# Kernel optimization log

Measured on AMD Instinct MI355X. Metric: run time of the kernel, lower is better.

## Reference

```python
import jax, jax.numpy as jnp
import numpy as np

NUM_GRAPHS = 512

def _segment_softmax(logits, seg, n):
    m = jax.ops.segment_max(logits, seg, num_segments=n)
    e = jnp.exp(logits - m[seg])
    z = jax.ops.segment_sum(e, seg, num_segments=n)
    return e / (z[seg] + 1e-16)

def _gat(x_src, x_dst, W_src, W_dst, a_src, a_dst, bias, src, dst, n_dst, n_loop):
    # PyG GATConv (concat=True, eval-mode dropout, self-loops added with
    # num_nodes = min(N_src, N_dst); inputs are guaranteed self-loop-free).
    H, C = a_src.shape
    hs = (x_src @ W_src).reshape(-1, H, C)  # [Ns,H,C]
    hd = (x_dst @ W_dst).reshape(-1, H, C)  # [Nd,H,C]
    als = jnp.einsum('nhc,hc->nh', hs, a_src)
    ald = jnp.einsum('nhc,hc->nh', hd, a_dst)
    loop = jnp.arange(n_loop)
    s = jnp.concatenate([src, loop])
    d = jnp.concatenate([dst, loop])
    logits = jax.nn.leaky_relu(als[s] + ald[d], 0.2)  # [E,H]
    alpha = _segment_softmax(logits, d, n_dst)
    out = jax.ops.segment_sum(hs[s] * alpha[:, :, None], d, num_segments=n_dst)
    return out.reshape(-1, H * C) + bias

def _graph_layernorm(x, batch, w, b, eps=1e-5):
    # PyG LayerNorm(mode='graph'): normalize over all nodes+features per graph.
    F = x.shape[-1]
    cnt = jax.ops.segment_sum(jnp.ones((x.shape[0],), x.dtype), batch, num_segments=NUM_GRAPHS)
    norm = jnp.maximum(cnt, 1.0) * F
    mean = jax.ops.segment_sum(x.sum(-1), batch, num_segments=NUM_GRAPHS) / norm
    xc = x - mean[batch][:, None]
    var = jax.ops.segment_sum((xc * xc).sum(-1), batch, num_segments=NUM_GRAPHS) / norm
    return xc * jax.lax.rsqrt(var + eps)[batch][:, None] * w + b

def _sag_pool(x, src, dst, batch, Wrel, brel, Wroot):
    # SAGPooling(min_score=-1): GraphConv score -> per-graph softmax; softmax>0>-1
    # so all nodes kept in order, x scaled by score.
    agg = jax.ops.segment_sum(x[src], dst, num_segments=x.shape[0])
    score = (agg @ Wrel + brel + x @ Wroot).reshape(-1)
    score = _segment_softmax(score, batch, NUM_GRAPHS)
    return x * score[:, None]

def setup_inputs() -> dict:
    key = jax.random.key(0)
    ks = jax.random.split(key, 32)
    N_ATOM, N_AA, B = 25600, 204800, 512
    E_ATOM, E_AA, E_M2P = 102400, 1024000, 512000
    D, H, C = 200, 2, 50
    HC = H * C
    sa = jax.random.randint(ks[0], (E_ATOM,), 0, N_ATOM)
    atom_edge_index = jnp.stack([sa, (sa + jax.random.randint(ks[1], (E_ATOM,), 1, N_ATOM)) % N_ATOM])
    sp = jax.random.randint(ks[2], (E_AA,), 0, N_AA)
    aa_edge_index = jnp.stack([sp, (sp + jax.random.randint(ks[3], (E_AA,), 1, N_AA)) % N_AA])
    m0 = jax.random.randint(ks[4], (E_M2P,), 0, N_ATOM)
    m1 = jax.random.randint(ks[5], (E_M2P,), 0, N_AA)
    m1 = jnp.where(m1 == m0, (m1 + 1) % N_AA, m1)  # keep bipartite edges self-loop-free
    m2p_edge_index = jnp.stack([m0, m1])
    f = lambda k, shape: jax.random.normal(k, shape, jnp.float32) * 0.05
    return dict(
        atom_x=jax.random.normal(ks[8], (N_ATOM, D)),
        atom_edge_index=atom_edge_index,
        atom_batch=jnp.sort(jax.random.randint(ks[6], (N_ATOM,), 0, B)),
        aa_x=jax.random.normal(ks[9], (N_AA, D)),
        aa_edge_index=aa_edge_index,
        aa_edge_attr=jax.random.uniform(ks[10], (E_AA, 1)),
        aa_batch=jnp.sort(jax.random.randint(ks[7], (N_AA,), 0, B)),
        m2p_edge_index=m2p_edge_index,
        Wd=f(ks[11], (D, HC)), ad_src=f(ks[12], (H, C)), ad_dst=f(ks[13], (H, C)), bd=jnp.zeros((HC,)),
        Wp=f(ks[14], (D, HC)), ap_src=f(ks[15], (H, C)), ap_dst=f(ks[16], (H, C)), bp=jnp.zeros((HC,)),
        Wi_src=f(ks[17], (D, HC)), Wi_dst=f(ks[18], (D, HC)), ai_src=f(ks[19], (H, C)), ai_dst=f(ks[20], (H, C)), bi=jnp.zeros((HC,)),
        ln_d_w=jnp.ones((D,)), ln_d_b=jnp.zeros((D,)),
        ln_p_w=jnp.ones((D,)), ln_p_b=jnp.zeros((D,)),
        pd_Wrel=f(ks[21], (D, 1)), pd_brel=jnp.zeros((1,)), pd_Wroot=f(ks[22], (D, 1)),
        pp_Wrel=f(ks[23], (D, 1)), pp_brel=jnp.zeros((1,)), pp_Wroot=f(ks[24], (D, 1)),
    )

def reference(atom_x, atom_edge_index, atom_batch, aa_x, aa_edge_index, aa_edge_attr, aa_batch, m2p_edge_index,
              Wd, ad_src, ad_dst, bd, Wp, ap_src, ap_dst, bp,
              Wi_src, Wi_dst, ai_src, ai_dst, bi,
              ln_d_w, ln_d_b, ln_p_w, ln_p_b,
              pd_Wrel, pd_brel, pd_Wroot, pp_Wrel, pp_brel, pp_Wroot):
    n_atom, n_aa = atom_x.shape[0], aa_x.shape[0]
    n_loop = min(n_atom, n_aa)
    atom_x = jax.nn.elu(atom_x)
    aa_x = jax.nn.elu(aa_x)
    # drug intra + inter (m2p flipped: src=aa, dst=atom)
    atom_intra = _gat(atom_x, atom_x, Wd, Wd, ad_src, ad_dst, bd,
                      atom_edge_index[0], atom_edge_index[1], n_atom, n_atom)
    atom_inter = _gat(aa_x, atom_x, Wi_src, Wi_dst, ai_src, ai_dst, bi,
                      m2p_edge_index[1], m2p_edge_index[0], n_atom, n_loop)
    atom_h = jax.nn.elu(_graph_layernorm(jnp.concatenate([atom_intra, atom_inter], -1), atom_batch, ln_d_w, ln_d_b))
    # protein intra + inter (uses UPDATED atom features; aa_edge_attr ignored: GATConv has no edge_dim)
    aa_intra = _gat(aa_x, aa_x, Wp, Wp, ap_src, ap_dst, bp,
                    aa_edge_index[0], aa_edge_index[1], n_aa, n_aa)
    aa_inter = _gat(atom_h, aa_x, Wi_src, Wi_dst, ai_src, ai_dst, bi,
                    m2p_edge_index[0], m2p_edge_index[1], n_aa, n_loop)
    aa_h = jax.nn.elu(_graph_layernorm(jnp.concatenate([aa_intra, aa_inter], -1), aa_batch, ln_p_w, ln_p_b))
    atom_out = _sag_pool(atom_h, atom_edge_index[0], atom_edge_index[1], atom_batch, pd_Wrel, pd_brel, pd_Wroot)
    aa_out = _sag_pool(aa_h, aa_edge_index[0], aa_edge_index[1], aa_batch, pp_Wrel, pp_brel, pp_Wroot)
    drug_g = jax.ops.segment_sum(atom_out, atom_batch, num_segments=NUM_GRAPHS)
    prot_g = jax.ops.segment_sum(aa_out, aa_batch, num_segments=NUM_GRAPHS)
    return atom_out, aa_out, drug_g, prot_g
```

## Files before the change

kernel.cpp:

```cpp
#include <hip/hip_runtime.h>

#define DF 200
#define HC 100
#define NH 2
#define CD 50
#define NG 512
#define SCB 256

__device__ __forceinline__ float eluf(float x){ return x>0.f ? x : expm1f(x); }

__device__ __forceinline__ void fma4(float4& a, float s, const float4& w){
  a.x += s*w.x; a.y += s*w.y; a.z += s*w.z; a.w += s*w.w;
}

__device__ __forceinline__ void seg_range(const int* __restrict__ batch, int N, int g,
                                          int& start, int& end){
  int lo=0, hi=N;
  while(lo<hi){ int m=(lo+hi)>>1; if(batch[m]<g) lo=m+1; else hi=m; }
  start=lo; hi=N;
  while(lo<hi){ int m=(lo+hi)>>1; if(batch[m]<g+1) lo=m+1; else hi=m; }
  end=lo;
}

__global__ void k_hist(const int* __restrict__ dst, int E, int* __restrict__ deg){
  int e = blockIdx.x*blockDim.x + threadIdx.x;
  if(e<E) atomicAdd(&deg[dst[e]], 1);
}

__global__ void k_scan1(int* __restrict__ a, int N, int* __restrict__ bsum){
  __shared__ int sh[SCB];
  int t = threadIdx.x, i = blockIdx.x*SCB + t;
  int v = (i<N)? a[i] : 0;
  sh[t] = v; __syncthreads();
  for(int o=1;o<SCB;o<<=1){
    int u = (t>=o)? sh[t-o] : 0; __syncthreads();
    sh[t] += u; __syncthreads();
  }
  if(i<N) a[i] = sh[t]-v;
  if(t==SCB-1) bsum[blockIdx.x] = sh[t];
}

__global__ void k_scan2(int* __restrict__ bsum, int nb){
  __shared__ int sh[1024];
  int t = threadIdx.x;
  int v = (t<nb)? bsum[t] : 0;
  sh[t]=v; __syncthreads();
  for(int o=1;o<1024;o<<=1){ int u=(t>=o)?sh[t-o]:0; __syncthreads(); sh[t]+=u; __syncthreads(); }
  if(t<nb) bsum[t] = sh[t]-v;
}

__global__ void k_scan3(int* __restrict__ rowptr, int* __restrict__ cursor,
                        const int* __restrict__ bsum, int N, int E){
  int i = blockIdx.x*SCB + threadIdx.x;
  if(i<N){ int v = rowptr[i] + bsum[blockIdx.x]; rowptr[i]=v; cursor[i]=v; }
  if(blockIdx.x==0 && threadIdx.x==0) rowptr[N]=E;
}

__global__ void k_fill(const int* __restrict__ src, const int* __restrict__ dst, int E,
                       int* __restrict__ cursor, int* __restrict__ csrc){
  int e = blockIdx.x*blockDim.x + threadIdx.x;
  if(e<E){ int p = atomicAdd(&cursor[dst[e]],1); csrc[p] = src[e]; }
}

__global__ void k_elu(const float* __restrict__ in, float* __restrict__ out, int n){
  int i = blockIdx.x*blockDim.x + threadIdx.x;
  if(i<n) out[i] = eluf(in[i]);
}

__global__ void k_makeV(const float* __restrict__ W, const float* __restrict__ a, float* __restrict__ V){
  int i = blockIdx.x*blockDim.x + threadIdx.x;
  if(i >= DF*NH) return;
  int k = i>>1, h = i&1;
  float s = 0.f;
  #pragma unroll
  for(int c=0;c<CD;c++) s += W[k*HC + h*CD + c] * a[h*CD + c];
  V[k*2+h] = s;
}

__global__ void k_pack2(const float* __restrict__ a, const float* __restrict__ c, float* __restrict__ V){
  int k = blockIdx.x*blockDim.x + threadIdx.x;
  if(k<DF){ V[k*2] = a[k]; V[k*2+1] = c[k]; }
}

__global__ void k_gemv3(const float* __restrict__ X,
                        const float* __restrict__ V0, const float* __restrict__ V1, const float* __restrict__ V2,
                        float* __restrict__ o0, float* __restrict__ o1, float* __restrict__ o2, int N){
  int n = blockIdx.x*4 + (threadIdx.x>>6);
  if(n>=N) return;
  int lane = threadIdx.x & 63;
  const float2* xr = (const float2*)(X + (size_t)n*DF);
  float a00=0,a01=0,a10=0,a11=0,a20=0,a21=0;
  for(int k2=lane;k2<DF/2;k2+=64){
    float2 x2 = xr[k2];
    float4 v0 = ((const float4*)V0)[k2];
    float4 v1 = ((const float4*)V1)[k2];
    float4 v2 = ((const float4*)V2)[k2];
    a00 += x2.x*v0.x + x2.y*v0.z;  a01 += x2.x*v0.y + x2.y*v0.w;
    a10 += x2.x*v1.x + x2.y*v1.z;  a11 += x2.x*v1.y + x2.y*v1.w;
    a20 += x2.x*v2.x + x2.y*v2.z;  a21 += x2.x*v2.y + x2.y*v2.w;
  }
  for(int o=32;o;o>>=1){
    a00+=__shfl_down(a00,o); a01+=__shfl_down(a01,o);
    a10+=__shfl_down(a10,o); a11+=__shfl_down(a11,o);
    a20+=__shfl_down(a20,o); a21+=__shfl_down(a21,o);
  }
  if(lane==0){
    o0[n*2]=a00; o0[n*2+1]=a01;
    o1[n*2]=a10; o1[n*2+1]=a11;
    o2[n*2]=a20; o2[n*2+1]=a21;
  }
}

__global__ void k_gemv4(const float* __restrict__ X,
                        const float* __restrict__ V0, const float* __restrict__ V1,
                        const float* __restrict__ V2, const float* __restrict__ V3,
                        float* __restrict__ o0, float* __restrict__ o1,
                        float* __restrict__ o2, float* __restrict__ o3, int N){
  int n = blockIdx.x*4 + (threadIdx.x>>6);
  if(n>=N) return;
  int lane = threadIdx.x & 63;
  const float2* xr = (const float2*)(X + (size_t)n*DF);
  float a00=0,a01=0,a10=0,a11=0,a20=0,a21=0,a30=0,a31=0;
  for(int k2=lane;k2<DF/2;k2+=64){
    float2 x2 = xr[k2];
    float4 v0 = ((const float4*)V0)[k2];
    float4 v1 = ((const float4*)V1)[k2];
    float4 v2 = ((const float4*)V2)[k2];
    float4 v3 = ((const float4*)V3)[k2];
    a00 += x2.x*v0.x + x2.y*v0.z;  a01 += x2.x*v0.y + x2.y*v0.w;
    a10 += x2.x*v1.x + x2.y*v1.z;  a11 += x2.x*v1.y + x2.y*v1.w;
    a20 += x2.x*v2.x + x2.y*v2.z;  a21 += x2.x*v2.y + x2.y*v2.w;
    a30 += x2.x*v3.x + x2.y*v3.z;  a31 += x2.x*v3.y + x2.y*v3.w;
  }
  for(int o=32;o;o>>=1){
    a00+=__shfl_down(a00,o); a01+=__shfl_down(a01,o);
    a10+=__shfl_down(a10,o); a11+=__shfl_down(a11,o);
    a20+=__shfl_down(a20,o); a21+=__shfl_down(a21,o);
    a30+=__shfl_down(a30,o); a31+=__shfl_down(a31,o);
  }
  if(lane==0){
    o0[n*2]=a00; o0[n*2+1]=a01;
    o1[n*2]=a10; o1[n*2+1]=a11;
    o2[n*2]=a20; o2[n*2+1]=a21;
    o3[n*2]=a30; o3[n*2+1]=a31;
  }
}

__global__ void k_gemm(const float* __restrict__ X, const float* __restrict__ W,
                       float* __restrict__ out, int N){
  int i = blockIdx.x*blockDim.x + threadIdx.x;
  int nq4 = (N+3)>>2;
  if(i >= nq4*25) return;
  int nq = i/25, cg = i%25;
  int n0 = nq*4;
  int r1 = min(n0+1,N-1), r2 = min(n0+2,N-1), r3 = min(n0+3,N-1);
  const float* x0 = X + (size_t)n0*DF;
  const float* x1 = X + (size_t)r1*DF;
  const float* x2 = X + (size_t)r2*DF;
  const float* x3 = X + (size_t)r3*DF;
  const float* wp = W + cg*4;
  float4 a0={0,0,0,0}, a1={0,0,0,0}, a2={0,0,0,0}, a3={0,0,0,0};
  for(int k=0;k<DF;k+=4){
    float4 xa = *(const float4*)(x0 + k);
    float4 xb = *(const float4*)(x1 + k);
    float4 xc = *(const float4*)(x2 + k);
    float4 xd = *(const float4*)(x3 + k);
    float4 w0 = *(const float4*)(wp + (k  )*HC);
    float4 w1 = *(const float4*)(wp + (k+1)*HC);
    float4 w2 = *(const float4*)(wp + (k+2)*HC);
    float4 w3 = *(const float4*)(wp + (k+3)*HC);
    fma4(a0,xa.x,w0); fma4(a0,xa.y,w1); fma4(a0,xa.z,w2); fma4(a0,xa.w,w3);
    fma4(a1,xb.x,w0); fma4(a1,xb.y,w1); fma4(a1,xb.z,w2); fma4(a1,xb.w,w3);
    fma4(a2,xc.x,w0); fma4(a2,xc.y,w1); fma4(a2,xc.z,w2); fma4(a2,xc.w,w3);
    fma4(a3,xd.x,w0); fma4(a3,xd.y,w1); fma4(a3,xd.z,w2); fma4(a3,xd.w,w3);
  }
  float* o = out + (size_t)n0*HC + cg*4;
  *(float4*)(o) = a0;
  if(n0+1<N) *(float4*)(o+HC)   = a1;
  if(n0+2<N) *(float4*)(o+2*HC) = a2;
  if(n0+3<N) *(float4*)(o+3*HC) = a3;
}

__global__ void k_gemm2(const float* __restrict__ X,
                        const float* __restrict__ W1, const float* __restrict__ W2,
                        float* __restrict__ out1, float* __restrict__ out2, int N){
  int i = blockIdx.x*blockDim.x + threadIdx.x;
  int nq4 = (N+3)>>2;
  if(i >= nq4*25) return;
  int nq = i/25, cg = i%25;
  int n0 = nq*4;
  int r1 = min(n0+1,N-1), r2 = min(n0+2,N-1), r3 = min(n0+3,N-1);
  const float* x0 = X + (size_t)n0*DF;
  const float* x1 = X + (size_t)r1*DF;
  const float* x2 = X + (size_t)r2*DF;
  const float* x3 = X + (size_t)r3*DF;
  const float* wp1 = W1 + cg*4;
  const float* wp2 = W2 + cg*4;
  float4 a0={0,0,0,0}, a1={0,0,0,0}, a2={0,0,0,0}, a3={0,0,0,0};
  float4 b0={0,0,0,0}, b1={0,0,0,0}, b2={0,0,0,0}, b3={0,0,0,0};
  for(int k=0;k<DF;k+=4){
    float4 xa = *(const float4*)(x0 + k);
    float4 xb = *(const float4*)(x1 + k);
    float4 xc = *(const float4*)(x2 + k);
    float4 xd = *(const float4*)(x3 + k);
    float4 u0 = *(const float4*)(wp1 + (k  )*HC);
    float4 u1 = *(const float4*)(wp1 + (k+1)*HC);
    float4 u2 = *(const float4*)(wp1 + (k+2)*HC);
    float4 u3 = *(const float4*)(wp1 + (k+3)*HC);
    float4 v0 = *(const float4*)(wp2 + (k  )*HC);
    float4 v1 = *(const float4*)(wp2 + (k+1)*HC);
    float4 v2 = *(const float4*)(wp2 + (k+2)*HC);
    float4 v3 = *(const float4*)(wp2 + (k+3)*HC);
    fma4(a0,xa.x,u0); fma4(a0,xa.y,u1); fma4(a0,xa.z,u2); fma4(a0,xa.w,u3);
    fma4(a1,xb.x,u0); fma4(a1,xb.y,u1); fma4(a1,xb.z,u2); fma4(a1,xb.w,u3);
    fma4(a2,xc.x,u0); fma4(a2,xc.y,u1); fma4(a2,xc.z,u2); fma4(a2,xc.w,u3);
    fma4(a3,xd.x,u0); fma4(a3,xd.y,u1); fma4(a3,xd.z,u2); fma4(a3,xd.w,u3);
    fma4(b0,xa.x,v0); fma4(b0,xa.y,v1); fma4(b0,xa.z,v2); fma4(b0,xa.w,v3);
    fma4(b1,xb.x,v0); fma4(b1,xb.y,v1); fma4(b1,xb.z,v2); fma4(b1,xb.w,v3);
    fma4(b2,xc.x,v0); fma4(b2,xc.y,v1); fma4(b2,xc.z,v2); fma4(b2,xc.w,v3);
    fma4(b3,xd.x,v0); fma4(b3,xd.y,v1); fma4(b3,xd.z,v2); fma4(b3,xd.w,v3);
  }
  float* o1 = out1 + (size_t)n0*HC + cg*4;
  float* o2 = out2 + (size_t)n0*HC + cg*4;
  *(float4*)(o1) = a0;
  *(float4*)(o2) = b0;
  if(n0+1<N){ *(float4*)(o1+HC)   = a1; *(float4*)(o2+HC)   = b1; }
  if(n0+2<N){ *(float4*)(o1+2*HC) = a2; *(float4*)(o2+2*HC) = b2; }
  if(n0+3<N){ *(float4*)(o1+3*HC) = a3; *(float4*)(o2+3*HC) = b3; }
}

__global__ void k_gat_gather(const int* __restrict__ rowptr, const int* __restrict__ csrc,
                             const float* __restrict__ hs,
                             const float* __restrict__ als, const float* __restrict__ ald,
                             const float* __restrict__ bias,
                             float* __restrict__ cat, int colOff, int nloop, int N){
  int n = blockIdx.x; if(n>=N) return;
  int f = threadIdx.x; if(f>=HC) return;
  int h = f/CD;
  float aldh = ald[n*2+h];
  float bi_f = bias[f];
  float acc = 0.f, z = 0.f;
  int e = rowptr[n], e1 = rowptr[n+1];
  for(; e<e1; e++){
    int s = csrc[e];
    float lg = als[s*2+h] + aldh;
    lg = lg>0.f ? lg : 0.2f*lg;
    float ev = __expf(lg);
    z += ev;
    acc += ev*hs[(size_t)s*HC+f];
  }
  if(n<nloop){
    float lg = als[n*2+h] + aldh;
    lg = lg>0.f ? lg : 0.2f*lg;
    float ev = __expf(lg);
    z += ev;
    acc += ev*hs[(size_t)n*HC+f];
  }
  cat[(size_t)n*DF + colOff + f] = acc/(z+1e-16f) + bi_f;
}

__global__ void k_ln_stats2(const float* __restrict__ cat, const int* __restrict__ batch,
                            float* __restrict__ gs, float* __restrict__ gq, float* __restrict__ gc, int N){
  int g = blockIdx.x, start, end;
  seg_range(batch, N, g, start, end);
  const float4* c4 = (const float4*)cat;
  int i0 = start*(DF/4), i1 = end*(DF/4);
  float s=0.f, q=0.f;
  for(int i=i0+threadIdx.x; i<i1; i+=blockDim.x){
    float4 v = c4[i];
    s += v.x+v.y+v.z+v.w;
    q += v.x*v.x+v.y*v.y+v.z*v.z+v.w*v.w;
  }
  for(int o=32;o;o>>=1){ s+=__shfl_down(s,o); q+=__shfl_down(q,o); }
  __shared__ float ss[8], sq[8];
  int wv = threadIdx.x>>6;
  if((threadIdx.x&63)==0){ ss[wv]=s; sq[wv]=q; }
  __syncthreads();
  if(threadIdx.x==0){
    float S=0.f, Q=0.f;
    int nw = blockDim.x>>6;
    for(int k=0;k<nw;k++){ S+=ss[k]; Q+=sq[k]; }
    gs[g]=S; gq[g]=Q; gc[g]=(float)(end-start);
  }
}

__global__ void k_ln_norm_f(float* __restrict__ x, const int* __restrict__ batch,
                            const float* __restrict__ gs, const float* __restrict__ gq, const float* __restrict__ gc,
                            const float* __restrict__ wv, const float* __restrict__ bv,
                            const float* __restrict__ V0, float* __restrict__ o0,
                            const float* __restrict__ V1, float* __restrict__ o1, int N){
  int n = blockIdx.x*4 + (threadIdx.x>>6);
  if(n>=N) return;
  int lane = threadIdx.x & 63;
  int g = batch[n];
  float norm = fmaxf(gc[g],1.f)*(float)DF;
  float mean = gs[g]/norm;
  float var  = fmaxf(gq[g]/norm - mean*mean, 0.f);
  float rs   = rsqrtf(var+1e-5f);
  float2* xr = (float2*)(x + (size_t)n*DF);
  float a00=0,a01=0,a10=0,a11=0;
  for(int k2=lane;k2<DF/2;k2+=64){
    float2 x2 = xr[k2];
    float2 w2 = ((const float2*)wv)[k2];
    float2 b2 = ((const float2*)bv)[k2];
    float v0 = eluf((x2.x-mean)*rs*w2.x + b2.x);
    float v1 = eluf((x2.y-mean)*rs*w2.y + b2.y);
    xr[k2] = make_float2(v0,v1);
    float4 vv = ((const float4*)V0)[k2];
    a00 += v0*vv.x + v1*vv.z;  a01 += v0*vv.y + v1*vv.w;
    if(V1){
      float4 u = ((const float4*)V1)[k2];
      a10 += v0*u.x + v1*u.z;  a11 += v0*u.y + v1*u.w;
    }
  }
  for(int o=32;o;o>>=1){
    a00+=__shfl_down(a00,o); a01+=__shfl_down(a01,o);
    a10+=__shfl_down(a10,o); a11+=__shfl_down(a11,o);
  }
  if(lane==0){
    o0[n*2]=a00; o0[n*2+1]=a01;
    if(o1){ o1[n*2]=a10; o1[n*2+1]=a11; }
  }
}

__global__ void k_sag_gather(const int* __restrict__ rowptr, const int* __restrict__ csrc,
                             const float* __restrict__ y2, float* __restrict__ sagg, int N){
  int n = blockIdx.x*blockDim.x + threadIdx.x;
  if(n>=N) return;
  float s=0.f;
  int e1 = rowptr[n+1];
  for(int e=rowptr[n]; e<e1; e++) s += y2[csrc[e]*2];
  sagg[n] = s;
}

__global__ void k_sag_exp(const float* __restrict__ sagg, const float* __restrict__ y2,
                          const float* __restrict__ brel,
                          float* __restrict__ en, float* __restrict__ zg,
                          const int* __restrict__ batch, int N){
  int n = blockIdx.x*blockDim.x + threadIdx.x;
  if(n>=N) return;
  float sc = sagg[n] + brel[0] + y2[n*2+1];
  float e = __expf(sc);
  en[n] = e;
  atomicAdd(&zg[batch[n]], e);
}

__global__ void k_sag_out(const float* __restrict__ x, const float* __restrict__ en,
                          const float* __restrict__ zg, const int* __restrict__ batch,
                          float* __restrict__ out, int N){
  int i = blockIdx.x*blockDim.x + threadIdx.x;
  if(i>=N*DF) return;
  int n = i/DF;
  float a = en[n]/(zg[batch[n]]+1e-16f);
  out[i] = x[i]*a;
}

__global__ void k_graph_sum(const float* __restrict__ x, const float* __restrict__ en,
                            const float* __restrict__ zg, const int* __restrict__ batch,
                            float* __restrict__ outg, int N){
  int g = blockIdx.x, start, end;
  seg_range(batch, N, g, start, end);
  int f = threadIdx.x;
  if(f>=DF) return;
  float s = 0.f;
  int n = start;
  for(; n+4<=end; n+=4){
    s += x[(size_t) n   *DF+f]*en[n]
       + x[(size_t)(n+1)*DF+f]*en[n+1]
       + x[(size_t)(n+2)*DF+f]*en[n+2]
       + x[(size_t)(n+3)*DF+f]*en[n+3];
  }
  for(; n<end; n++) s += x[(size_t)n*DF+f]*en[n];
  outg[(size_t)g*DF+f] = s/(zg[g]+1e-16f);
}

extern "C" void kernel_launch(void* const* d_in, const int* in_sizes, int n_in,
                              void* d_out, int out_size, void* d_ws, size_t ws_size,
                              hipStream_t stream){
  const float* atom_x    = (const float*)d_in[0];
  const int*   atom_ei   = (const int*)  d_in[1];
  const int*   atom_batch= (const int*)  d_in[2];
  const float* aa_x      = (const float*)d_in[3];
  const int*   aa_ei     = (const int*)  d_in[4];
  const int*   aa_batch  = (const int*)  d_in[6];
  const int*   m2p       = (const int*)  d_in[7];
  const float* Wd     =(const float*)d_in[8];
  const float* ad_src =(const float*)d_in[9];
  const float* ad_dst =(const float*)d_in[10];
  const float* bd     =(const float*)d_in[11];
  const float* Wp     =(const float*)d_in[12];
  const float* ap_src =(const float*)d_in[13];
  const float* ap_dst =(const float*)d_in[14];
  const float* bp     =(const float*)d_in[15];
  const float* Wi_src =(const float*)d_in[16];
  const float* Wi_dst =(const float*)d_in[17];
  const float* ai_src =(const float*)d_in[18];
  const float* ai_dst =(const float*)d_in[19];
  const float* bi     =(const float*)d_in[20];
  const float* ln_d_w =(const float*)d_in[21];
  const float* ln_d_b =(const float*)d_in[22];
  const float* ln_p_w =(const float*)d_in[23];
  const float* ln_p_b =(const float*)d_in[24];
  const float* pd_Wrel=(const float*)d_in[25];
  const float* pd_brel=(const float*)d_in[26];
  const float* pd_Wroot=(const float*)d_in[27];
  const float* pp_Wrel=(const float*)d_in[28];
  const float* pp_brel=(const float*)d_in[29];
  const float* pp_Wroot=(const float*)d_in[30];

  const int nA = in_sizes[0]/DF;
  const int EA = in_sizes[1]/2;
  const int nP = in_sizes[3]/DF;
  const int EP = in_sizes[4]/2;
  const int EM = in_sizes[7]/2;
  const int nLoop = nA<nP ? nA : nP;

  float* w = (float*)d_ws;
  size_t off = 0;
  auto alloc = [&](size_t n){ float* p = w+off; off += (n+63)&~(size_t)63; return p; };

  float* AX  = alloc((size_t)nA*DF);
  float* AB  = alloc((size_t)nP*DF);
  float* H1  = alloc((size_t)nA*HC);
  float* HS2 = alloc((size_t)nP*HC);
  float* H3  = alloc((size_t)nP*HC);
  float* als1=alloc((size_t)nA*2); float* ald1=alloc((size_t)nA*2);
  float* als2=alloc((size_t)nP*2); float* ald2=alloc((size_t)nA*2);
  float* als3=alloc((size_t)nP*2); float* ald3=alloc((size_t)nP*2);
  float* als4=alloc((size_t)nA*2); float* ald4=alloc((size_t)nP*2);
  float* Vds=alloc(DF*2); float* Vdd=alloc(DF*2);
  float* Vps=alloc(DF*2); float* Vpd=alloc(DF*2);
  float* Vis=alloc(DF*2); float* Vid=alloc(DF*2);
  float* VsA=alloc(DF*2); float* VsP=alloc(DF*2);
  float* y2A=alloc((size_t)nA*2); float* y2P=alloc((size_t)nP*2);
  float* enA=alloc(nA);   float* enP=alloc(nP);
  float* gsA=alloc(NG); float* gqA=alloc(NG); float* gcA=alloc(NG);
  float* gsP=alloc(NG); float* gqP=alloc(NG); float* gcP=alloc(NG);
  float* saggA=alloc(nA); float* saggP=alloc(nP);
  int* srcAi = (int*)alloc(EA);
  int* srcAm = (int*)alloc(EM);
  int* srcPi = (int*)alloc(EP);
  int* srcPm = (int*)alloc(EM);
  int* curAi = (int*)alloc(nA); int* curAm = (int*)alloc(nA);
  int* curPi = (int*)alloc(nP); int* curPm = (int*)alloc(nP);
  int* bsum  = (int*)alloc(1024);
  float* zr0 = w+off;
  int* rpAi = (int*)alloc(nA+1); int* rpAm = (int*)alloc(nA+1);
  int* rpPi = (int*)alloc(nP+1); int* rpPm = (int*)alloc(nP+1);
  float* zgA=alloc(NG); float* zgP=alloc(NG);
  size_t zrBytes = ((w+off) - zr0)*sizeof(float);
  if(off*sizeof(float) > ws_size) return;

  float* out_atom = (float*)d_out;
  float* out_aa   = out_atom + (size_t)nA*DF;
  float* out_dg   = out_aa   + (size_t)nP*DF;
  float* out_pg   = out_dg   + (size_t)NG*DF;

  const int B = 256;
  hipMemsetAsync(zr0, 0, zrBytes, stream);

  auto buildCSR = [&](const int* esrc, const int* edst, int E, int N,
                      int* rowptr, int* cursor, int* csrc){
    int nb = (N+SCB-1)/SCB;
    k_hist <<<(E+B-1)/B, B, 0, stream>>>(edst, E, rowptr);
    k_scan1<<<nb, SCB, 0, stream>>>(rowptr, N, bsum);
    k_scan2<<<1, 1024, 0, stream>>>(bsum, nb);
    k_scan3<<<nb, SCB, 0, stream>>>(rowptr, cursor, bsum, N, E);
    k_fill <<<(E+B-1)/B, B, 0, stream>>>(esrc, edst, E, cursor, csrc);
  };
  buildCSR(atom_ei,      atom_ei+EA, EA, nA, rpAi, curAi, srcAi);
  buildCSR(m2p+EM,       m2p,        EM, nA, rpAm, curAm, srcAm);
  buildCSR(aa_ei,        aa_ei+EP,   EP, nP, rpPi, curPi, srcPi);
  buildCSR(m2p,          m2p+EM,     EM, nP, rpPm, curPm, srcPm);

  k_elu<<<(nA*DF+B-1)/B, B, 0, stream>>>(atom_x, AX, nA*DF);
  k_elu<<<(nP*DF+B-1)/B, B, 0, stream>>>(aa_x,   AB, nP*DF);

  k_makeV<<<2,B,0,stream>>>(Wd,     ad_src, Vds);
  k_makeV<<<2,B,0,stream>>>(Wd,     ad_dst, Vdd);
  k_makeV<<<2,B,0,stream>>>(Wp,     ap_src, Vps);
  k_makeV<<<2,B,0,stream>>>(Wp,     ap_dst, Vpd);
  k_makeV<<<2,B,0,stream>>>(Wi_src, ai_src, Vis);
  k_makeV<<<2,B,0,stream>>>(Wi_dst, ai_dst, Vid);
  k_pack2<<<1,B,0,stream>>>(pd_Wrel, pd_Wroot, VsA);
  k_pack2<<<1,B,0,stream>>>(pp_Wrel, pp_Wroot, VsP);

  { int tot = ((nA+3)/4)*25;
    k_gemm<<<(tot+B-1)/B, B, 0, stream>>>(AX, Wd, H1, nA); }
  { int tot = ((nP+3)/4)*25;
    k_gemm2<<<(tot+B-1)/B, B, 0, stream>>>(AB, Wi_src, Wp, HS2, H3, nP); }
  k_gemv3<<<(nA+3)/4,B,0,stream>>>(AX, Vds, Vdd, Vid, als1, ald1, ald2, nA);
  k_gemv4<<<(nP+3)/4,B,0,stream>>>(AB, Vis, Vps, Vpd, Vid, als2, als3, ald3, ald4, nP);

  k_gat_gather<<<nA,128,0,stream>>>(rpAi, srcAi, H1,  als1, ald1, bd, AX, 0,  nA,    nA);
  k_gat_gather<<<nA,128,0,stream>>>(rpAm, srcAm, HS2, als2, ald2, bi, AX, HC, nLoop, nA);
  k_gat_gather<<<nP,128,0,stream>>>(rpPi, srcPi, H3,  als3, ald3, bp, AB, 0,  nP,    nP);

  k_ln_stats2<<<NG,512,0,stream>>>(AX, atom_batch, gsA, gqA, gcA, nA);
  k_ln_norm_f<<<(nA+3)/4,B,0,stream>>>(AX, atom_batch, gsA, gqA, gcA, ln_d_w, ln_d_b,
                                       Vis, als4, VsA, y2A, nA);

  { int tot = ((nA+3)/4)*25;
    k_gemm<<<(tot+B-1)/B, B, 0, stream>>>(AX, Wi_src, H1, nA); }
  k_gat_gather<<<nP,128,0,stream>>>(rpPm, srcPm, H1, als4, ald4, bi, AB, HC, nLoop, nP);

  k_ln_stats2<<<NG,512,0,stream>>>(AB, aa_batch, gsP, gqP, gcP, nP);
  k_ln_norm_f<<<(nP+3)/4,B,0,stream>>>(AB, aa_batch, gsP, gqP, gcP, ln_p_w, ln_p_b,
                                       VsP, y2P, (const float*)nullptr, (float*)nullptr, nP);

  k_sag_gather<<<(nA+B-1)/B,B,0,stream>>>(rpAi, srcAi, y2A, saggA, nA);
  k_sag_exp<<<(nA+B-1)/B,B,0,stream>>>(saggA, y2A, pd_brel, enA, zgA, atom_batch, nA);
  k_sag_out<<<(nA*DF+B-1)/B,B,0,stream>>>(AX, enA, zgA, atom_batch, out_atom, nA);
  k_graph_sum<<<NG,B,0,stream>>>(AX, enA, zgA, atom_batch, out_dg, nA);

  k_sag_gather<<<(nP+B-1)/B,B,0,stream>>>(rpPi, srcPi, y2P, saggP, nP);
  k_sag_exp<<<(nP+B-1)/B,B,0,stream>>>(saggP, y2P, pp_brel, enP, zgP, aa_batch, nP);
  k_sag_out<<<(nP*DF+B-1)/B,B,0,stream>>>(AB, enP, zgP, aa_batch, out_aa, nP);
  k_graph_sum<<<NG,B,0,stream>>>(AB, enP, zgP, aa_batch, out_pg, nP);
}
```

Before: 2.484 ms.

## Fuse input ELU into GEMM/GEMV loads and stage X tiles in LDS

```diff
diff --git a/kernel.cpp b/kernel.cpp
--- a/kernel.cpp
+++ b/kernel.cpp
@@ -6,6 +6,8 @@
 #define CD 50
 #define NG 512
 #define SCB 256
+#define TM 40
+#define XLD (DF+4)
 
 __device__ __forceinline__ float eluf(float x){ return x>0.f ? x : expm1f(x); }
 
@@ -60,11 +62,6 @@
                        int* __restrict__ cursor, int* __restrict__ csrc){
   int e = blockIdx.x*blockDim.x + threadIdx.x;
   if(e<E){ int p = atomicAdd(&cursor[dst[e]],1); csrc[p] = src[e]; }
-}
-
-__global__ void k_elu(const float* __restrict__ in, float* __restrict__ out, int n){
-  int i = blockIdx.x*blockDim.x + threadIdx.x;
-  if(i<n) out[i] = eluf(in[i]);
 }
 
 __global__ void k_makeV(const float* __restrict__ W, const float* __restrict__ a, float* __restrict__ V){
@@ -92,6 +89,7 @@
   float a00=0,a01=0,a10=0,a11=0,a20=0,a21=0;
   for(int k2=lane;k2<DF/2;k2+=64){
     float2 x2 = xr[k2];
+    x2.x = eluf(x2.x); x2.y = eluf(x2.y);
     float4 v0 = ((const float4*)V0)[k2];
     float4 v1 = ((const float4*)V1)[k2];
     float4 v2 = ((const float4*)V2)[k2];
@@ -123,6 +121,7 @@
   float a00=0,a01=0,a10=0,a11=0,a20=0,a21=0,a30=0,a31=0;
   for(int k2=lane;k2<DF/2;k2+=64){
     float2 x2 = xr[k2];
+    x2.x = eluf(x2.x); x2.y = eluf(x2.y);
     float4 v0 = ((const float4*)V0)[k2];
     float4 v1 = ((const float4*)V1)[k2];
     float4 v2 = ((const float4*)V2)[k2];
@@ -146,18 +145,29 @@
   }
 }
 
-__global__ void k_gemm(const float* __restrict__ X, const float* __restrict__ W,
-                       float* __restrict__ out, int N){
-  int i = blockIdx.x*blockDim.x + threadIdx.x;
-  int nq4 = (N+3)>>2;
-  if(i >= nq4*25) return;
+template<int ELU>
+__global__ __launch_bounds__(256) void k_gemm_t(const float* __restrict__ X, const float* __restrict__ W,
+                                                float* __restrict__ out, int N){
+  __shared__ float xs[TM*XLD];
+  int bm = blockIdx.x*TM;
+  int rows = min(TM, N-bm);
+  for(int idx = threadIdx.x; idx < rows*(DF/4); idx += blockDim.x){
+    int r = idx/(DF/4), c = idx%(DF/4);
+    float4 v = *(const float4*)(X + (size_t)(bm+r)*DF + c*4);
+    if(ELU){ v.x=eluf(v.x); v.y=eluf(v.y); v.z=eluf(v.z); v.w=eluf(v.w); }
+    *(float4*)(&xs[r*XLD + c*4]) = v;
+  }
+  __syncthreads();
+  int i = threadIdx.x;
+  if(i >= 250) return;
   int nq = i/25, cg = i%25;
   int n0 = nq*4;
-  int r1 = min(n0+1,N-1), r2 = min(n0+2,N-1), r3 = min(n0+3,N-1);
-  const float* x0 = X + (size_t)n0*DF;
-  const float* x1 = X + (size_t)r1*DF;
-  const float* x2 = X + (size_t)r2*DF;
-  const float* x3 = X + (size_t)r3*DF;
+  if(n0 >= rows) return;
+  int r1 = min(n0+1,rows-1), r2 = min(n0+2,rows-1), r3 = min(n0+3,rows-1);
+  const float* x0 = xs + n0*XLD;
+  const float* x1 = xs + r1*XLD;
+  const float* x2 = xs + r2*XLD;
+  const float* x3 = xs + r3*XLD;
   const float* wp = W + cg*4;
   float4 a0={0,0,0,0}, a1={0,0,0,0}, a2={0,0,0,0}, a3={0,0,0,0};
   for(int k=0;k<DF;k+=4){
@@ -174,26 +184,37 @@
     fma4(a2,xc.x,w0); fma4(a2,xc.y,w1); fma4(a2,xc.z,w2); fma4(a2,xc.w,w3);
     fma4(a3,xd.x,w0); fma4(a3,xd.y,w1); fma4(a3,xd.z,w2); fma4(a3,xd.w,w3);
   }
-  float* o = out + (size_t)n0*HC + cg*4;
+  float* o = out + (size_t)(bm+n0)*HC + cg*4;
   *(float4*)(o) = a0;
-  if(n0+1<N) *(float4*)(o+HC)   = a1;
-  if(n0+2<N) *(float4*)(o+2*HC) = a2;
-  if(n0+3<N) *(float4*)(o+3*HC) = a3;
-}
-
-__global__ void k_gemm2(const float* __restrict__ X,
+  if(n0+1<rows) *(float4*)(o+HC)   = a1;
+  if(n0+2<rows) *(float4*)(o+2*HC) = a2;
+  if(n0+3<rows) *(float4*)(o+3*HC) = a3;
+}
+
+template<int ELU>
+__global__ __launch_bounds__(256) void k_gemm2_t(const float* __restrict__ X,
                         const float* __restrict__ W1, const float* __restrict__ W2,
                         float* __restrict__ out1, float* __restrict__ out2, int N){
-  int i = blockIdx.x*blockDim.x + threadIdx.x;
-  int nq4 = (N+3)>>2;
-  if(i >= nq4*25) return;
+  __shared__ float xs[TM*XLD];
+  int bm = blockIdx.x*TM;
+  int rows = min(TM, N-bm);
+  for(int idx = threadIdx.x; idx < rows*(DF/4); idx += blockDim.x){
+    int r = idx/(DF/4), c = idx%(DF/4);
+    float4 v = *(const float4*)(X + (size_t)(bm+r)*DF + c*4);
+    if(ELU){ v.x=eluf(v.x); v.y=eluf(v.y); v.z=eluf(v.z); v.w=eluf(v.w); }
+    *(float4*)(&xs[r*XLD + c*4]) = v;
+  }
+  __syncthreads();
+  int i = threadIdx.x;
+  if(i >= 250) return;
   int nq = i/25, cg = i%25;
   int n0 = nq*4;
-  int r1 = min(n0+1,N-1), r2 = min(n0+2,N-1), r3 = min(n0+3,N-1);
-  const float* x0 = X + (size_t)n0*DF;
-  const float* x1 = X + (size_t)r1*DF;
-  const float* x2 = X + (size_t)r2*DF;
-  const float* x3 = X + (size_t)r3*DF;
+  if(n0 >= rows) return;
+  int r1 = min(n0+1,rows-1), r2 = min(n0+2,rows-1), r3 = min(n0+3,rows-1);
+  const float* x0 = xs + n0*XLD;
+  const float* x1 = xs + r1*XLD;
+  const float* x2 = xs + r2*XLD;
+  const float* x3 = xs + r3*XLD;
   const float* wp1 = W1 + cg*4;
   const float* wp2 = W2 + cg*4;
   float4 a0={0,0,0,0}, a1={0,0,0,0}, a2={0,0,0,0}, a3={0,0,0,0};
@@ -220,13 +241,13 @@
     fma4(b2,xc.x,v0); fma4(b2,xc.y,v1); fma4(b2,xc.z,v2); fma4(b2,xc.w,v3);
     fma4(b3,xd.x,v0); fma4(b3,xd.y,v1); fma4(b3,xd.z,v2); fma4(b3,xd.w,v3);
   }
-  float* o1 = out1 + (size_t)n0*HC + cg*4;
-  float* o2 = out2 + (size_t)n0*HC + cg*4;
+  float* o1 = out1 + (size_t)(bm+n0)*HC + cg*4;
+  float* o2 = out2 + (size_t)(bm+n0)*HC + cg*4;
   *(float4*)(o1) = a0;
   *(float4*)(o2) = b0;
-  if(n0+1<N){ *(float4*)(o1+HC)   = a1; *(float4*)(o2+HC)   = b1; }
-  if(n0+2<N){ *(float4*)(o1+2*HC) = a2; *(float4*)(o2+2*HC) = b2; }
-  if(n0+3<N){ *(float4*)(o1+3*HC) = a3; *(float4*)(o2+3*HC) = b3; }
+  if(n0+1<rows){ *(float4*)(o1+HC)   = a1; *(float4*)(o2+HC)   = b1; }
+  if(n0+2<rows){ *(float4*)(o1+2*HC) = a2; *(float4*)(o2+2*HC) = b2; }
+  if(n0+3<rows){ *(float4*)(o1+3*HC) = a3; *(float4*)(o2+3*HC) = b3; }
 }
 
 __global__ void k_gat_gather(const int* __restrict__ rowptr, const int* __restrict__ csrc,
@@ -473,9 +494,6 @@
   buildCSR(aa_ei,        aa_ei+EP,   EP, nP, rpPi, curPi, srcPi);
   buildCSR(m2p,          m2p+EM,     EM, nP, rpPm, curPm, srcPm);
 
-  k_elu<<<(nA*DF+B-1)/B, B, 0, stream>>>(atom_x, AX, nA*DF);
-  k_elu<<<(nP*DF+B-1)/B, B, 0, stream>>>(aa_x,   AB, nP*DF);
-
   k_makeV<<<2,B,0,stream>>>(Wd,     ad_src, Vds);
   k_makeV<<<2,B,0,stream>>>(Wd,     ad_dst, Vdd);
   k_makeV<<<2,B,0,stream>>>(Wp,     ap_src, Vps);
@@ -485,12 +503,10 @@
   k_pack2<<<1,B,0,stream>>>(pd_Wrel, pd_Wroot, VsA);
   k_pack2<<<1,B,0,stream>>>(pp_Wrel, pp_Wroot, VsP);
 
-  { int tot = ((nA+3)/4)*25;
-    k_gemm<<<(tot+B-1)/B, B, 0, stream>>>(AX, Wd, H1, nA); }
-  { int tot = ((nP+3)/4)*25;
-    k_gemm2<<<(tot+B-1)/B, B, 0, stream>>>(AB, Wi_src, Wp, HS2, H3, nP); }
-  k_gemv3<<<(nA+3)/4,B,0,stream>>>(AX, Vds, Vdd, Vid, als1, ald1, ald2, nA);
-  k_gemv4<<<(nP+3)/4,B,0,stream>>>(AB, Vis, Vps, Vpd, Vid, als2, als3, ald3, ald4, nP);
+  k_gemm_t<1><<<(nA+TM-1)/TM, B, 0, stream>>>(atom_x, Wd, H1, nA);
+  k_gemm2_t<1><<<(nP+TM-1)/TM, B, 0, stream>>>(aa_x, Wi_src, Wp, HS2, H3, nP);
+  k_gemv3<<<(nA+3)/4,B,0,stream>>>(atom_x, Vds, Vdd, Vid, als1, ald1, ald2, nA);
+  k_gemv4<<<(nP+3)/4,B,0,stream>>>(aa_x, Vis, Vps, Vpd, Vid, als2, als3, ald3, ald4, nP);
 
   k_gat_gather<<<nA,128,0,stream>>>(rpAi, srcAi, H1,  als1, ald1, bd, AX, 0,  nA,    nA);
   k_gat_gather<<<nA,128,0,stream>>>(rpAm, srcAm, HS2, als2, ald2, bi, AX, HC, nLoop, nA);
@@ -500,8 +516,7 @@
   k_ln_norm_f<<<(nA+3)/4,B,0,stream>>>(AX, atom_batch, gsA, gqA, gcA, ln_d_w, ln_d_b,
                                        Vis, als4, VsA, y2A, nA);
 
-  { int tot = ((nA+3)/4)*25;
-    k_gemm<<<(tot+B-1)/B, B, 0, stream>>>(AX, Wi_src, H1, nA); }
+  k_gemm_t<0><<<(nA+TM-1)/TM, B, 0, stream>>>(AX, Wi_src, H1, nA);
   k_gat_gather<<<nP,128,0,stream>>>(rpPm, srcPm, H1, als4, ald4, bi, AB, HC, nLoop, nP);
 
   k_ln_stats2<<<NG,512,0,stream>>>(AB, aa_batch, gsP, gqP, gcP, nP);
```

New measurement: 2.139 ms. 13.9% less time.
